# Optimization experiments

Hardware: AMD Instinct MI355X
Metric: run time of the kernel (lower is better)

The kernel has to match this reference:

```python
import jax, jax.numpy as jnp
import numpy as np

N = 100000   # nodes
E = 1600000  # edges
IN = 128
HID = 128    # 2 * out_channels
OUT = 64


def setup_inputs() -> dict:
    key = jax.random.key(0)
    ks = jax.random.split(key, 8)
    x = jax.random.normal(ks[0], (N, IN), dtype=jnp.float32)
    edge_index = jax.random.randint(ks[1], (2, E), 0, N, dtype=jnp.int32)
    s = 1.0 / np.sqrt(IN)
    W1 = jax.random.normal(ks[2], (IN, HID), dtype=jnp.float32) * s
    Wm1 = jax.random.normal(ks[3], (HID, HID), dtype=jnp.float32) * s
    Wm2 = jax.random.normal(ks[4], (HID, HID), dtype=jnp.float32) * s
    W2 = jax.random.normal(ks[5], (HID, OUT), dtype=jnp.float32) * s
    b1 = jnp.zeros((HID,), jnp.float32)
    bm1 = jnp.zeros((HID,), jnp.float32)
    bm2 = jnp.zeros((HID,), jnp.float32)
    b2 = jnp.zeros((OUT,), jnp.float32)
    return {"x": x, "edge_index": edge_index, "W1": W1, "b1": b1,
            "Wm1": Wm1, "bm1": bm1, "Wm2": Wm2, "bm2": bm2,
            "W2": W2, "b2": b2}


def _gcn_norm(edge_index, num_nodes):
    # PyG GCNConv: add self-loops (weight 1), symmetric normalization.
    loop = jnp.arange(num_nodes, dtype=edge_index.dtype)
    src = jnp.concatenate([edge_index[0], loop])
    dst = jnp.concatenate([edge_index[1], loop])
    deg = jax.ops.segment_sum(jnp.ones_like(src, jnp.float32), dst,
                              num_segments=num_nodes)
    dinv = jnp.where(deg > 0, jax.lax.rsqrt(deg), 0.0)
    norm = dinv[src] * dinv[dst]  # [E + N]
    return src, dst, norm


def _gcn_conv(h, W, b, src, dst, norm, num_nodes):
    h = h @ W                                # dense transform [N, F_out]
    msg = h[src] * norm[:, None]             # gather + scale   [E+N, F_out]
    out = jax.ops.segment_sum(msg, dst, num_segments=num_nodes)  # scatter-add
    return out + b


def reference(x, edge_index, W1, b1, Wm1, bm1, Wm2, bm2, W2, b2):
    num_nodes = x.shape[0]
    src, dst, norm = _gcn_norm(edge_index, num_nodes)
    h = jax.nn.relu(_gcn_conv(x, W1, b1, src, dst, norm, num_nodes))
    h = jax.nn.relu(_gcn_conv(h, Wm1, bm1, src, dst, norm, num_nodes))
    h = jax.nn.relu(_gcn_conv(h, Wm2, bm2, src, dst, norm, num_nodes))
    return _gcn_conv(h, W2, b2, src, dst, norm, num_nodes)  # [N, OUT]
```

## Files before the change

kernel.cpp:

```cpp
#include <hip/hip_runtime.h>
#include <hip/hip_bf16.h>
#include <hip/hip_fp16.h>


#define NNODES 100000
#define NEDGES 1600000
#define NBUCK 782

typedef __attribute__((ext_vector_type(8))) short bf16x8;
typedef __attribute__((ext_vector_type(4))) float f32x4;


__device__ inline float2 h2f2(unsigned int u) {
    __half2 h = *reinterpret_cast<__half2*>(&u);
    return __half22float2(h);
}
__device__ inline unsigned int f22h2(float a, float b) {
    __half2 h = __floats2half2_rn(a, b);
    return *reinterpret_cast<unsigned int*>(&h);
}

__device__ inline void split1(float x, short& hi, short& lo) {
    unsigned int u = __float_as_uint(x);
    hi = (short)(u >> 16);
    float r = x - __uint_as_float(u & 0xFFFF0000u);
    lo = (short)(__float_as_uint(r) >> 16);
}

__device__ inline void split8f(const float* f, bf16x8& hi, bf16x8& lo) {
#pragma unroll
    for (int i = 0; i < 8; i++) { short h, l; split1(f[i], h, l); hi[i] = h; lo[i] = l; }
}


__global__ void zero_ints(int* p, int n) {
    int i = blockIdx.x * blockDim.x + threadIdx.x;
    if (i < n) p[i] = 0;
}

__global__ __launch_bounds__(256) void hist_pass(const int* __restrict__ dst,
                                                 int* __restrict__ cnt, int e) {
    __shared__ int h[NBUCK];
    int tid = threadIdx.x;
    for (int i = tid; i < NBUCK; i += 256) h[i] = 0;
    __syncthreads();
    int base_e = blockIdx.x * 4096;
#pragma unroll
    for (int j = 0; j < 16; j++) {
        int i = base_e + j * 256 + tid;
        if (i < e) atomicAdd(&h[dst[i] >> 7], 1);
    }
    __syncthreads();
    for (int b = tid; b < NBUCK; b += 256)
        if (h[b]) atomicAdd(&cnt[b], h[b]);
}

__global__ __launch_bounds__(256) void scan_buckets(const int* __restrict__ cnt,
                                                    int* __restrict__ base,
                                                    int* __restrict__ fill, int e) {
    __shared__ int sd[256];
    int t = threadIdx.x;
    int v[4]; int s = 0;
#pragma unroll
    for (int j = 0; j < 4; j++) {
        int i = t * 4 + j;
        v[j] = (i < NBUCK) ? cnt[i] : 0;
        s += v[j];
    }
    sd[t] = s; __syncthreads();
    for (int off = 1; off < 256; off <<= 1) {
        int x = (t >= off) ? sd[t - off] : 0;
        __syncthreads();
        sd[t] += x;
        __syncthreads();
    }
    int run = sd[t] - s;
#pragma unroll
    for (int j = 0; j < 4; j++) {
        int i = t * 4 + j;
        if (i < NBUCK) { base[i] = run; fill[i] = run; }
        run += v[j];
    }
    if (t == 0) base[NBUCK] = e;
}

__global__ __launch_bounds__(256) void scatter_pass(const int* __restrict__ src,
                                                    const int* __restrict__ dst,
                                                    int* __restrict__ fill,
                                                    unsigned int* __restrict__ epart, int e) {
    __shared__ int h[NBUCK];
    int tid = threadIdx.x;
    for (int i = tid; i < NBUCK; i += 256) h[i] = 0;
    __syncthreads();
    int base_e = blockIdx.x * 4096;
#pragma unroll
    for (int j = 0; j < 16; j++) {
        int i = base_e + j * 256 + tid;
        if (i < e) atomicAdd(&h[dst[i] >> 7], 1);
    }
    __syncthreads();
    for (int b = tid; b < NBUCK; b += 256)
        if (h[b]) h[b] = atomicAdd(&fill[b], h[b]);
    __syncthreads();
#pragma unroll
    for (int j = 0; j < 16; j++) {
        int i = base_e + j * 256 + tid;
        if (i < e) {
            int d = dst[i];
            int bk = d >> 7;
            int pos = atomicAdd(&h[bk], 1);
            epart[pos] = ((unsigned int)src[i] << 7) | (unsigned int)(d & 127);
        }
    }
}

__global__ __launch_bounds__(256) void build_csr(const unsigned int* __restrict__ epart,
                                                 const int* __restrict__ base,
                                                 int* __restrict__ row_ptr,
                                                 int* __restrict__ col,
                                                 float* __restrict__ dinv,
                                                 int n, int e_total) {
    __shared__ int deg[128], off[128], fil[128];
    int b = blockIdx.x, tid = threadIdx.x;
    int node0 = b << 7;
    int nn = n - node0; if (nn > 128) nn = 128;
    int e0 = base[b], e1 = base[b + 1];
    int cnt = e1 - e0;

    if (tid < 128) deg[tid] = 0;
    __syncthreads();
    for (int i = tid; i < cnt; i += 256)
        atomicAdd(&deg[epart[e0 + i] & 127], 1);
    __syncthreads();
    if (tid < 128) off[tid] = deg[tid];
    __syncthreads();
    for (int o = 1; o < 128; o <<= 1) {
        int x = (tid < 128 && tid >= o) ? off[tid - o] : 0;
        __syncthreads();
        if (tid < 128) off[tid] += x;
        __syncthreads();
    }
    if (tid < nn) {
        int ex = e0 + off[tid] - deg[tid];
        row_ptr[node0 + tid] = ex;
        fil[tid] = ex;
        dinv[node0 + tid] = rsqrtf((float)(deg[tid] + 1));
    }
    if (b == 0 && tid == 0) row_ptr[n] = e_total;
    __syncthreads();
    for (int i = tid; i < cnt; i += 256) {
        unsigned int u = epart[e0 + i];
        int ld = (int)(u & 127);
        int pos = atomicAdd(&fil[ld], 1);
        col[pos] = (int)(u >> 7);
    }
}


__device__ inline void wfrag_one(const float* W, unsigned short* hi, unsigned short* lo,
                                 int e, int NT, int Ncols) {
    int j = e & 7;
    int l = (e >> 3) & 63;
    int t = (e >> 9) % NT;
    int c = e / (512 * NT);
    int k = c * 32 + (l >> 4) * 8 + j;
    int n = t * 16 + (l & 15);
    float x = W[k * Ncols + n];
    short h, lw; split1(x, h, lw);
    hi[e] = (unsigned short)h;
    lo[e] = (unsigned short)lw;
}

__global__ void conv_all(const float* W1, unsigned short* hi1, unsigned short* lo1,
                         const float* Wm1, unsigned short* him1, unsigned short* lom1,
                         const float* Wm2, unsigned short* him2, unsigned short* lom2,
                         const float* W2, unsigned short* hi2, unsigned short* lo2) {
    int blk = blockIdx.x;
    int tid = threadIdx.x;
    if (blk < 64)        wfrag_one(W1,  hi1,  lo1,  blk * 256 + tid,        8, 128);
    else if (blk < 128)  wfrag_one(Wm1, him1, lom1, (blk - 64) * 256 + tid, 8, 128);
    else if (blk < 192)  wfrag_one(Wm2, him2, lom2, (blk - 128) * 256 + tid, 8, 128);
    else                 wfrag_one(W2,  hi2,  lo2,  (blk - 192) * 256 + tid, 4, 64);
}


template <typename AT, int BN>
__global__ __launch_bounds__(256) void gemm_mfma(const AT* __restrict__ A,
                                                 const unsigned short* __restrict__ gwhi,
                                                 const unsigned short* __restrict__ gwlo,
                                                 const float* __restrict__ dinv,
                                                 __half* __restrict__ T, int nrows) {
    constexpr int NT = BN / 16;
    constexpr int WFRAG = 4 * NT * 64 * 8;
    __shared__ __align__(16) unsigned short s_hi[WFRAG];
    __shared__ __align__(16) unsigned short s_lo[WFRAG];
    int tid = threadIdx.x;
    for (int i = tid; i < WFRAG / 8; i += 256) {
        ((uint4*)s_hi)[i] = ((const uint4*)gwhi)[i];
        ((uint4*)s_lo)[i] = ((const uint4*)gwlo)[i];
    }
    __syncthreads();

    int wave = tid >> 6, lane = tid & 63;
    int m = lane & 15, q = lane >> 4;
    long row0 = ((long)blockIdx.x * 4 + wave) * 32;
    if (row0 >= nrows) return;
    long rowa = row0 + m;
    bool hasb = (row0 + 16) < nrows;
    long rowb = hasb ? (row0 + 16 + m) : rowa;

    f32x4 acc[2][NT];
#pragma unroll
    for (int s = 0; s < 2; s++)
#pragma unroll
        for (int t = 0; t < NT; t++)
#pragma unroll
            for (int r = 0; r < 4; r++) acc[s][t][r] = 0.f;

#pragma unroll
    for (int c = 0; c < 4; c++) {
        bf16x8 ah[2], al[2];
        float fa[8], fb[8];
        if constexpr (sizeof(AT) == 2) {
            uint4 ra = *(const uint4*)((const __half*)A + rowa * 128 + c * 32 + q * 8);
            uint4 rb = *(const uint4*)((const __half*)A + rowb * 128 + c * 32 + q * 8);
            float2 t0;
            t0 = h2f2(ra.x); fa[0] = t0.x; fa[1] = t0.y;
            t0 = h2f2(ra.y); fa[2] = t0.x; fa[3] = t0.y;
            t0 = h2f2(ra.z); fa[4] = t0.x; fa[5] = t0.y;
            t0 = h2f2(ra.w); fa[6] = t0.x; fa[7] = t0.y;
            t0 = h2f2(rb.x); fb[0] = t0.x; fb[1] = t0.y;
            t0 = h2f2(rb.y); fb[2] = t0.x; fb[3] = t0.y;
            t0 = h2f2(rb.z); fb[4] = t0.x; fb[5] = t0.y;
            t0 = h2f2(rb.w); fb[6] = t0.x; fb[7] = t0.y;
        } else {
            const float* pa = (const float*)A + rowa * 128 + c * 32 + q * 8;
            const float* pb = (const float*)A + rowb * 128 + c * 32 + q * 8;
            *(float4*)&fa[0] = *(const float4*)pa;
            *(float4*)&fa[4] = *(const float4*)(pa + 4);
            *(float4*)&fb[0] = *(const float4*)pb;
            *(float4*)&fb[4] = *(const float4*)(pb + 4);
        }
        split8f(fa, ah[0], al[0]);
        split8f(fb, ah[1], al[1]);

#pragma unroll
        for (int t = 0; t < NT; t++) {
            bf16x8 bhi = *(const bf16x8*)(s_hi + ((c * NT + t) * 64 + lane) * 8);
            bf16x8 blo = *(const bf16x8*)(s_lo + ((c * NT + t) * 64 + lane) * 8);
#pragma unroll
            for (int s = 0; s < 2; s++) {
                acc[s][t] = __builtin_amdgcn_mfma_f32_16x16x32_bf16(al[s], bhi, acc[s][t], 0, 0, 0);
                acc[s][t] = __builtin_amdgcn_mfma_f32_16x16x32_bf16(ah[s], blo, acc[s][t], 0, 0, 0);
                acc[s][t] = __builtin_amdgcn_mfma_f32_16x16x32_bf16(ah[s], bhi, acc[s][t], 0, 0, 0);
            }
        }
    }

#pragma unroll
    for (int s = 0; s < 2; s++) {
        if (s == 1 && !hasb) break;
#pragma unroll
        for (int r = 0; r < 4; r++) {
            long row = row0 + s * 16 + q * 4 + r;
            if (row < nrows) {
                float di = dinv[row];
#pragma unroll
                for (int t = 0; t < NT; t++)
                    T[row * BN + t * 16 + m] = __float2half(acc[s][t][r] * di);
            }
        }
    }
}


__device__ inline void acc8(float* a, uint4 v) {
    float2 f0 = h2f2(v.x), f1 = h2f2(v.y), f2 = h2f2(v.z), f3 = h2f2(v.w);
    a[0] += f0.x; a[1] += f0.y; a[2] += f1.x; a[3] += f1.y;
    a[4] += f2.x; a[5] += f2.y; a[6] += f3.x; a[7] += f3.y;
}
__device__ inline void acc4(float* a, uint2 v) {
    float2 f0 = h2f2(v.x), f1 = h2f2(v.y);
    a[0] += f0.x; a[1] += f0.y; a[2] += f1.x; a[3] += f1.y;
}

__global__ __launch_bounds__(256) void agg128h(const __half* __restrict__ t,
                                               const int* __restrict__ row_ptr,
                                               const int* __restrict__ col,
                                               const float* __restrict__ dinv,
                                               const float* __restrict__ bias,
                                               __half* __restrict__ out, int n) {
    int wave = threadIdx.x >> 6, lane = threadIdx.x & 63;
    int node = blockIdx.x * 4 + wave;
    if (node >= n) return;
    int q = lane >> 4, i = lane & 15;
    int r0 = row_ptr[node], r1 = row_ptr[node + 1];
    const uint4* t4 = (const uint4*)t;

    float a0[8], a1[8], a2[8], a3[8];
#pragma unroll
    for (int k = 0; k < 8; k++) { a0[k] = 0.f; a1[k] = 0.f; a2[k] = 0.f; a3[k] = 0.f; }

    int p = r0;
    for (; p + 16 <= r1; p += 16) {
        int c0 = col[p + q];
        int c1 = col[p + 4 + q];
        int c2 = col[p + 8 + q];
        int c3 = col[p + 12 + q];
        uint4 v0 = t4[(size_t)c0 * 16 + i];
        uint4 v1 = t4[(size_t)c1 * 16 + i];
        uint4 v2 = t4[(size_t)c2 * 16 + i];
        uint4 v3 = t4[(size_t)c3 * 16 + i];
        acc8(a0, v0); acc8(a1, v1); acc8(a2, v2); acc8(a3, v3);
    }
    for (; p + 8 <= r1; p += 8) {
        int c0 = col[p + q];
        int c1 = col[p + 4 + q];
        uint4 v0 = t4[(size_t)c0 * 16 + i];
        uint4 v1 = t4[(size_t)c1 * 16 + i];
        acc8(a0, v0); acc8(a1, v1);
    }
    for (; p < r1; p += 4) {
        int idx = p + q;
        if (idx < r1) {
            int c = col[idx];
            acc8(a0, t4[(size_t)c * 16 + i]);
        }
    }

    float s[8];
#pragma unroll
    for (int k = 0; k < 8; k++) s[k] = (a0[k] + a1[k]) + (a2[k] + a3[k]);
#pragma unroll
    for (int k = 0; k < 8; k++) s[k] += __shfl_xor(s[k], 16);
#pragma unroll
    for (int k = 0; k < 8; k++) s[k] += __shfl_xor(s[k], 32);

    if (q == 0) {
        uint4 ownv = t4[(size_t)node * 16 + i];
        float own[8];
        float2 f0 = h2f2(ownv.x), f1 = h2f2(ownv.y), f2 = h2f2(ownv.z), f3 = h2f2(ownv.w);
        own[0] = f0.x; own[1] = f0.y; own[2] = f1.x; own[3] = f1.y;
        own[4] = f2.x; own[5] = f2.y; own[6] = f3.x; own[7] = f3.y;
        float di = dinv[node];
        float4 bA = ((const float4*)bias)[i * 2];
        float4 bB = ((const float4*)bias)[i * 2 + 1];
        float o[8];
        o[0] = di * (s[0] + own[0]) + bA.x;
        o[1] = di * (s[1] + own[1]) + bA.y;
        o[2] = di * (s[2] + own[2]) + bA.z;
        o[3] = di * (s[3] + own[3]) + bA.w;
        o[4] = di * (s[4] + own[4]) + bB.x;
        o[5] = di * (s[5] + own[5]) + bB.y;
        o[6] = di * (s[6] + own[6]) + bB.z;
        o[7] = di * (s[7] + own[7]) + bB.w;
#pragma unroll
        for (int k = 0; k < 8; k++) o[k] = fmaxf(o[k], 0.f);
        uint4 ov;
        ov.x = f22h2(o[0], o[1]); ov.y = f22h2(o[2], o[3]);
        ov.z = f22h2(o[4], o[5]); ov.w = f22h2(o[6], o[7]);
        ((uint4*)out)[(size_t)node * 16 + i] = ov;
    }
}

__global__ __launch_bounds__(256) void agg64h(const __half* __restrict__ t,
                                              const int* __restrict__ row_ptr,
                                              const int* __restrict__ col,
                                              const float* __restrict__ dinv,
                                              const float* __restrict__ bias,
                                              float* __restrict__ out, int n) {
    int wave = threadIdx.x >> 6, lane = threadIdx.x & 63;
    int node = blockIdx.x * 4 + wave;
    if (node >= n) return;
    int q = lane >> 4, i = lane & 15;
    int r0 = row_ptr[node], r1 = row_ptr[node + 1];
    const uint2* t2 = (const uint2*)t;

    float a0[4], a1[4], a2[4], a3[4];
#pragma unroll
    for (int k = 0; k < 4; k++) { a0[k] = 0.f; a1[k] = 0.f; a2[k] = 0.f; a3[k] = 0.f; }

    int p = r0;
    for (; p + 16 <= r1; p += 16) {
        int c0 = col[p + q];
        int c1 = col[p + 4 + q];
        int c2 = col[p + 8 + q];
        int c3 = col[p + 12 + q];
        uint2 v0 = t2[(size_t)c0 * 16 + i];
        uint2 v1 = t2[(size_t)c1 * 16 + i];
        uint2 v2 = t2[(size_t)c2 * 16 + i];
        uint2 v3 = t2[(size_t)c3 * 16 + i];
        acc4(a0, v0); acc4(a1, v1); acc4(a2, v2); acc4(a3, v3);
    }
    for (; p + 8 <= r1; p += 8) {
        int c0 = col[p + q];
        int c1 = col[p + 4 + q];
        uint2 v0 = t2[(size_t)c0 * 16 + i];
        uint2 v1 = t2[(size_t)c1 * 16 + i];
        acc4(a0, v0); acc4(a1, v1);
    }
    for (; p < r1; p += 4) {
        int idx = p + q;
        if (idx < r1) {
            int c = col[idx];
            acc4(a0, t2[(size_t)c * 16 + i]);
        }
    }

    float s[4];
#pragma unroll
    for (int k = 0; k < 4; k++) s[k] = (a0[k] + a1[k]) + (a2[k] + a3[k]);
#pragma unroll
    for (int k = 0; k < 4; k++) s[k] += __shfl_xor(s[k], 16);
#pragma unroll
    for (int k = 0; k < 4; k++) s[k] += __shfl_xor(s[k], 32);

    if (q == 0) {
        uint2 ownv = t2[(size_t)node * 16 + i];
        float own[4];
        float2 f0 = h2f2(ownv.x), f1 = h2f2(ownv.y);
        own[0] = f0.x; own[1] = f0.y; own[2] = f1.x; own[3] = f1.y;
        float di = dinv[node];
        float4 b4 = ((const float4*)bias)[i];
        float4 o;
        o.x = di * (s[0] + own[0]) + b4.x;
        o.y = di * (s[1] + own[1]) + b4.y;
        o.z = di * (s[2] + own[2]) + b4.z;
        o.w = di * (s[3] + own[3]) + b4.w;
        ((float4*)out)[(size_t)node * 16 + i] = o;
    }
}


extern "C" void kernel_launch(void* const* d_in, const int* in_sizes, int n_in,
                              void* d_out, int out_size, void* d_ws, size_t ws_size,
                              hipStream_t stream) {
    const int N = NNODES, E = NEDGES;
    const float* x   = (const float*)d_in[0];
    const int*   ei  = (const int*)d_in[1];
    const int*   src = ei;
    const int*   dst = ei + E;
    const float* W1  = (const float*)d_in[2];
    const float* b1  = (const float*)d_in[3];
    const float* Wm1 = (const float*)d_in[4];
    const float* bm1 = (const float*)d_in[5];
    const float* Wm2 = (const float*)d_in[6];
    const float* bm2 = (const float*)d_in[7];
    const float* W2  = (const float*)d_in[8];
    const float* b2  = (const float*)d_in[9];
    float* out = (float*)d_out;

    int* bucket_cnt  = (int*)d_ws;
    int* bucket_base = bucket_cnt + 784;
    int* bucket_fill = bucket_base + 784;
    int* row_ptr     = bucket_fill + 784;
    int* col         = row_ptr + (N + 4);
    unsigned int* epart = (unsigned int*)(col + E);
    float* dinv  = (float*)(epart + E);
    __half* t16  = (__half*)(dinv + N);
    __half* bufA = t16 + (size_t)N * 128;
    unsigned short* whi1  = (unsigned short*)(bufA + (size_t)N * 128);
    unsigned short* wlo1  = whi1 + 16384;
    unsigned short* whiM1 = wlo1 + 16384;
    unsigned short* wloM1 = whiM1 + 16384;
    unsigned short* whiM2 = wloM1 + 16384;
    unsigned short* wloM2 = whiM2 + 16384;
    unsigned short* whi2  = wloM2 + 16384;
    unsigned short* wlo2  = whi2 + 8192;

    const int EB4 = (E + 4095) / 4096;

    zero_ints<<<4, 256, 0, stream>>>(bucket_cnt, NBUCK);
    hist_pass<<<EB4, 256, 0, stream>>>(dst, bucket_cnt, E);
    scan_buckets<<<1, 256, 0, stream>>>(bucket_cnt, bucket_base, bucket_fill, E);
    scatter_pass<<<EB4, 256, 0, stream>>>(src, dst, bucket_fill, epart, E);
    build_csr<<<NBUCK, 256, 0, stream>>>(epart, bucket_base, row_ptr, col, dinv, N, E);

    conv_all<<<224, 256, 0, stream>>>(W1, whi1, wlo1, Wm1, whiM1, wloM1,
                                      Wm2, whiM2, wloM2, W2, whi2, wlo2);

    const int GB = (N + 127) / 128;
    const int AB = (N + 3) / 4;

    gemm_mfma<float, 128><<<GB, 256, 0, stream>>>(x, whi1, wlo1, dinv, t16, N);
    agg128h<<<AB, 256, 0, stream>>>(t16, row_ptr, col, dinv, b1, bufA, N);

    gemm_mfma<__half, 128><<<GB, 256, 0, stream>>>(bufA, whiM1, wloM1, dinv, t16, N);
    agg128h<<<AB, 256, 0, stream>>>(t16, row_ptr, col, dinv, bm1, bufA, N);

    gemm_mfma<__half, 128><<<GB, 256, 0, stream>>>(bufA, whiM2, wloM2, dinv, t16, N);
    agg128h<<<AB, 256, 0, stream>>>(t16, row_ptr, col, dinv, bm2, bufA, N);

    gemm_mfma<__half, 64><<<GB, 256, 0, stream>>>(bufA, whi2, wlo2, dinv, t16, N);
    agg64h<<<AB, 256, 0, stream>>>(t16, row_ptr, col, dinv, b2, out, N);
}
```

Measured before the change: 557.3 us.

## Switch GEMMs to fp16 split MFMA, fuse weight prep with scan, enlarge agg blocks

Replaces the bf16 hi/lo split GEMMs with fp16 MFMA. Hidden layers now feed the fp16 activations straight in, using two MFMAs instead of three with no float conversion or split; the first layer keeps a three-MFMA fp16 split. The bucket scan is merged into the weight-conversion kernel, with a small copy_fill kernel added. build_csr now orders each row's columns into low and high source halves, which may improve gather locality. Aggregation kernels move to 1024-thread blocks with 16 nodes per block. The fp16 split of weights narrows exponent range but is likely fine for these scales.

After: 620.4 us. 1.11x slower.

```diff
diff --git a/kernel.cpp b/kernel.cpp
--- a/kernel.cpp
+++ b/kernel.cpp
@@ -7,7 +7,7 @@
 #define NEDGES 1600000
 #define NBUCK 782
 
-typedef __attribute__((ext_vector_type(8))) short bf16x8;
+typedef __attribute__((ext_vector_type(8))) _Float16 f16x8;
 typedef __attribute__((ext_vector_type(4))) float f32x4;
 
 
@@ -20,16 +20,9 @@
     return *reinterpret_cast<unsigned int*>(&h);
 }
 
-__device__ inline void split1(float x, short& hi, short& lo) {
-    unsigned int u = __float_as_uint(x);
-    hi = (short)(u >> 16);
-    float r = x - __uint_as_float(u & 0xFFFF0000u);
-    lo = (short)(__float_as_uint(r) >> 16);
-}
-
-__device__ inline void split8f(const float* f, bf16x8& hi, bf16x8& lo) {
-#pragma unroll
-    for (int i = 0; i < 8; i++) { short h, l; split1(f[i], h, l); hi[i] = h; lo[i] = l; }
+__device__ inline void split_h(float x, __half& h, __half& l) {
+    h = __float2half(x);
+    l = __float2half(x - __half2float(h));
 }
 
 
@@ -54,108 +47,6 @@
     for (int b = tid; b < NBUCK; b += 256)
         if (h[b]) atomicAdd(&cnt[b], h[b]);
 }
-
-__global__ __launch_bounds__(256) void scan_buckets(const int* __restrict__ cnt,
-                                                    int* __restrict__ base,
-                                                    int* __restrict__ fill, int e) {
-    __shared__ int sd[256];
-    int t = threadIdx.x;
-    int v[4]; int s = 0;
-#pragma unroll
-    for (int j = 0; j < 4; j++) {
-        int i = t * 4 + j;
-        v[j] = (i < NBUCK) ? cnt[i] : 0;
-        s += v[j];
-    }
-    sd[t] = s; __syncthreads();
-    for (int off = 1; off < 256; off <<= 1) {
-        int x = (t >= off) ? sd[t - off] : 0;
-        __syncthreads();
-        sd[t] += x;
-        __syncthreads();
-    }
-    int run = sd[t] - s;
-#pragma unroll
-    for (int j = 0; j < 4; j++) {
-        int i = t * 4 + j;
-        if (i < NBUCK) { base[i] = run; fill[i] = run; }
-        run += v[j];
-    }
-    if (t == 0) base[NBUCK] = e;
-}
-
-__global__ __launch_bounds__(256) void scatter_pass(const int* __restrict__ src,
-                                                    const int* __restrict__ dst,
-                                                    int* __restrict__ fill,
-                                                    unsigned int* __restrict__ epart, int e) {
-    __shared__ int h[NBUCK];
-    int tid = threadIdx.x;
-    for (int i = tid; i < NBUCK; i += 256) h[i] = 0;
-    __syncthreads();
-    int base_e = blockIdx.x * 4096;
-#pragma unroll
-    for (int j = 0; j < 16; j++) {
-        int i = base_e + j * 256 + tid;
-        if (i < e) atomicAdd(&h[dst[i] >> 7], 1);
-    }
-    __syncthreads();
-    for (int b = tid; b < NBUCK; b += 256)
-        if (h[b]) h[b] = atomicAdd(&fill[b], h[b]);
-    __syncthreads();
-#pragma unroll
-    for (int j = 0; j < 16; j++) {
-        int i = base_e + j * 256 + tid;
-        if (i < e) {
-            int d = dst[i];
-            int bk = d >> 7;
-            int pos = atomicAdd(&h[bk], 1);
-            epart[pos] = ((unsigned int)src[i] << 7) | (unsigned int)(d & 127);
-        }
-    }
-}
-
-__global__ __launch_bounds__(256) void build_csr(const unsigned int* __restrict__ epart,
-                                                 const int* __restrict__ base,
-                                                 int* __restrict__ row_ptr,
-                                                 int* __restrict__ col,
-                                                 float* __restrict__ dinv,
-                                                 int n, int e_total) {
-    __shared__ int deg[128], off[128], fil[128];
-    int b = blockIdx.x, tid = threadIdx.x;
-    int node0 = b << 7;
-    int nn = n - node0; if (nn > 128) nn = 128;
-    int e0 = base[b], e1 = base[b + 1];
-    int cnt = e1 - e0;
-
-    if (tid < 128) deg[tid] = 0;
-    __syncthreads();
-    for (int i = tid; i < cnt; i += 256)
-        atomicAdd(&deg[epart[e0 + i] & 127], 1);
-    __syncthreads();
-    if (tid < 128) off[tid] = deg[tid];
-    __syncthreads();
-    for (int o = 1; o < 128; o <<= 1) {
-        int x = (tid < 128 && tid >= o) ? off[tid - o] : 0;
-        __syncthreads();
-        if (tid < 128) off[tid] += x;
-        __syncthreads();
-    }
-    if (tid < nn) {
-        int ex = e0 + off[tid] - deg[tid];
-        row_ptr[node0 + tid] = ex;
-        fil[tid] = ex;
-        dinv[node0 + tid] = rsqrtf((float)(deg[tid] + 1));
-    }
-    if (b == 0 && tid == 0) row_ptr[n] = e_total;
-    __syncthreads();
-    for (int i = tid; i < cnt; i += 256) {
-        unsigned int u = epart[e0 + i];
-        int ld = (int)(u & 127);
-        int pos = atomicAdd(&fil[ld], 1);
-        col[pos] = (int)(u >> 7);
-    }
-}
-
 
 __device__ inline void wfrag_one(const float* W, unsigned short* hi, unsigned short* lo,
                                  int e, int NT, int Ncols) {
@@ -166,30 +57,220 @@
     int k = c * 32 + (l >> 4) * 8 + j;
     int n = t * 16 + (l & 15);
     float x = W[k * Ncols + n];
-    short h, lw; split1(x, h, lw);
-    hi[e] = (unsigned short)h;
-    lo[e] = (unsigned short)lw;
-}
-
-__global__ void conv_all(const float* W1, unsigned short* hi1, unsigned short* lo1,
-                         const float* Wm1, unsigned short* him1, unsigned short* lom1,
-                         const float* Wm2, unsigned short* him2, unsigned short* lom2,
-                         const float* W2, unsigned short* hi2, unsigned short* lo2) {
+    __half h, lw; split_h(x, h, lw);
+    hi[e] = *(unsigned short*)&h;
+    lo[e] = *(unsigned short*)&lw;
+}
+
+__global__ __launch_bounds__(256) void aux_kernel(
+        const float* W1, unsigned short* hi1, unsigned short* lo1,
+        const float* Wm1, unsigned short* him1, unsigned short* lom1,
+        const float* Wm2, unsigned short* him2, unsigned short* lom2,
+        const float* W2, unsigned short* hi2, unsigned short* lo2,
+        const int* __restrict__ cnt, int* __restrict__ base, int e) {
     int blk = blockIdx.x;
     int tid = threadIdx.x;
-    if (blk < 64)        wfrag_one(W1,  hi1,  lo1,  blk * 256 + tid,        8, 128);
-    else if (blk < 128)  wfrag_one(Wm1, him1, lom1, (blk - 64) * 256 + tid, 8, 128);
-    else if (blk < 192)  wfrag_one(Wm2, him2, lom2, (blk - 128) * 256 + tid, 8, 128);
-    else                 wfrag_one(W2,  hi2,  lo2,  (blk - 192) * 256 + tid, 4, 64);
-}
-
-
-template <typename AT, int BN>
-__global__ __launch_bounds__(256) void gemm_mfma(const AT* __restrict__ A,
-                                                 const unsigned short* __restrict__ gwhi,
-                                                 const unsigned short* __restrict__ gwlo,
-                                                 const float* __restrict__ dinv,
-                                                 __half* __restrict__ T, int nrows) {
+    if (blk < 64)        { wfrag_one(W1,  hi1,  lo1,  blk * 256 + tid,         8, 128); return; }
+    if (blk < 128)       { wfrag_one(Wm1, him1, lom1, (blk - 64) * 256 + tid,  8, 128); return; }
+    if (blk < 192)       { wfrag_one(Wm2, him2, lom2, (blk - 128) * 256 + tid, 8, 128); return; }
+    if (blk < 224)       { wfrag_one(W2,  hi2,  lo2,  (blk - 192) * 256 + tid, 4, 64);  return; }
+    __shared__ int sd[256];
+    int t = tid;
+    int v[4]; int s = 0;
+#pragma unroll
+    for (int j = 0; j < 4; j++) {
+        int i = t * 4 + j;
+        v[j] = (i < NBUCK) ? cnt[i] : 0;
+        s += v[j];
+    }
+    sd[t] = s; __syncthreads();
+    for (int off = 1; off < 256; off <<= 1) {
+        int x = (t >= off) ? sd[t - off] : 0;
+        __syncthreads();
+        sd[t] += x;
+        __syncthreads();
+    }
+    int run = sd[t] - s;
+#pragma unroll
+    for (int j = 0; j < 4; j++) {
+        int i = t * 4 + j;
+        if (i < NBUCK) base[i] = run;
+        run += v[j];
+    }
+    if (t == 0) base[NBUCK] = e;
+}
+
+__global__ void copy_fill(const int* __restrict__ base, int* __restrict__ fill) {
+    int i = blockIdx.x * blockDim.x + threadIdx.x;
+    if (i < NBUCK) fill[i] = base[i];
+}
+
+__global__ __launch_bounds__(256) void scatter_pass(const int* __restrict__ src,
+                                                    const int* __restrict__ dst,
+                                                    int* __restrict__ fill,
+                                                    unsigned int* __restrict__ epart, int e) {
+    __shared__ int h[NBUCK];
+    int tid = threadIdx.x;
+    for (int i = tid; i < NBUCK; i += 256) h[i] = 0;
+    __syncthreads();
+    int base_e = blockIdx.x * 4096;
+#pragma unroll
+    for (int j = 0; j < 16; j++) {
+        int i = base_e + j * 256 + tid;
+        if (i < e) atomicAdd(&h[dst[i] >> 7], 1);
+    }
+    __syncthreads();
+    for (int b = tid; b < NBUCK; b += 256)
+        if (h[b]) h[b] = atomicAdd(&fill[b], h[b]);
+    __syncthreads();
+#pragma unroll
+    for (int j = 0; j < 16; j++) {
+        int i = base_e + j * 256 + tid;
+        if (i < e) {
+            int d = dst[i];
+            int bk = d >> 7;
+            int pos = atomicAdd(&h[bk], 1);
+            epart[pos] = ((unsigned int)src[i] << 7) | (unsigned int)(d & 127);
+        }
+    }
+}
+
+__global__ __launch_bounds__(256) void build_csr(const unsigned int* __restrict__ epart,
+                                                 const int* __restrict__ base,
+                                                 int* __restrict__ row_ptr,
+                                                 int* __restrict__ col,
+                                                 float* __restrict__ dinv,
+                                                 int n, int e_total) {
+    __shared__ int deg[128], degl[128], off[128], fil[256];
+    int b = blockIdx.x, tid = threadIdx.x;
+    int node0 = b << 7;
+    int nn = n - node0; if (nn > 128) nn = 128;
+    int e0 = base[b], e1 = base[b + 1];
+    int cnt = e1 - e0;
+    const int HALF = NNODES / 2;
+
+    if (tid < 128) { deg[tid] = 0; degl[tid] = 0; }
+    __syncthreads();
+    for (int i = tid; i < cnt; i += 256) {
+        unsigned int u = epart[e0 + i];
+        int ld = (int)(u & 127);
+        atomicAdd(&deg[ld], 1);
+        if ((int)(u >> 7) < HALF) atomicAdd(&degl[ld], 1);
+    }
+    __syncthreads();
+    if (tid < 128) off[tid] = deg[tid];
+    __syncthreads();
+    for (int o = 1; o < 128; o <<= 1) {
+        int x = (tid < 128 && tid >= o) ? off[tid - o] : 0;
+        __syncthreads();
+        if (tid < 128) off[tid] += x;
+        __syncthreads();
+    }
+    if (tid < 128) {
+        int row_start = e0 + off[tid] - deg[tid];
+        fil[tid] = row_start;
+        fil[128 + tid] = row_start + degl[tid];
+        if (tid < nn) {
+            row_ptr[node0 + tid] = row_start;
+            dinv[node0 + tid] = rsqrtf((float)(deg[tid] + 1));
+        }
+    }
+    if (b == 0 && tid == 0) row_ptr[n] = e_total;
+    __syncthreads();
+    for (int i = tid; i < cnt; i += 256) {
+        unsigned int u = epart[e0 + i];
+        int ld = (int)(u & 127);
+        int srcv = (int)(u >> 7);
+        int pos = atomicAdd(&fil[(srcv < HALF ? 0 : 128) + ld], 1);
+        col[pos] = srcv;
+    }
+}
+
+
+__global__ __launch_bounds__(256) void gemm_l1(const float* __restrict__ A,
+                                               const unsigned short* __restrict__ gwhi,
+                                               const unsigned short* __restrict__ gwlo,
+                                               const float* __restrict__ dinv,
+                                               __half* __restrict__ T, int nrows) {
+    constexpr int NT = 8, BN = 128;
+    constexpr int WFRAG = 4 * NT * 64 * 8;
+    __shared__ __align__(16) unsigned short s_hi[WFRAG];
+    __shared__ __align__(16) unsigned short s_lo[WFRAG];
+    int tid = threadIdx.x;
+    for (int i = tid; i < WFRAG / 8; i += 256) {
+        ((uint4*)s_hi)[i] = ((const uint4*)gwhi)[i];
+        ((uint4*)s_lo)[i] = ((const uint4*)gwlo)[i];
+    }
+    __syncthreads();
+
+    int wave = tid >> 6, lane = tid & 63;
+    int m = lane & 15, q = lane >> 4;
+    long row0 = ((long)blockIdx.x * 4 + wave) * 32;
+    if (row0 >= nrows) return;
+    long rowa = row0 + m;
+    bool hasb = (row0 + 16) < nrows;
+    long rowb = hasb ? (row0 + 16 + m) : rowa;
+
+    f32x4 acc[2][NT];
+#pragma unroll
+    for (int s = 0; s < 2; s++)
+#pragma unroll
+        for (int t = 0; t < NT; t++)
+#pragma unroll
+            for (int r = 0; r < 4; r++) acc[s][t][r] = 0.f;
+
+#pragma unroll
+    for (int c = 0; c < 4; c++) {
+        f16x8 ah[2], al[2];
+        const float* pa = A + rowa * 128 + c * 32 + q * 8;
+        const float* pb = A + rowb * 128 + c * 32 + q * 8;
+        float fa[8], fb[8];
+        *(float4*)&fa[0] = *(const float4*)pa;
+        *(float4*)&fa[4] = *(const float4*)(pa + 4);
+        *(float4*)&fb[0] = *(const float4*)pb;
+        *(float4*)&fb[4] = *(const float4*)(pb + 4);
+#pragma unroll
+        for (int i = 0; i < 8; i++) {
+            __half h, l;
+            split_h(fa[i], h, l); ah[0][i] = *(_Float16*)&h; al[0][i] = *(_Float16*)&l;
+            split_h(fb[i], h, l); ah[1][i] = *(_Float16*)&h; al[1][i] = *(_Float16*)&l;
+        }
+#pragma unroll
+        for (int t = 0; t < NT; t++) {
+            f16x8 bhi = *(const f16x8*)(s_hi + ((c * NT + t) * 64 + lane) * 8);
+            f16x8 blo = *(const f16x8*)(s_lo + ((c * NT + t) * 64 + lane) * 8);
+#pragma unroll
+            for (int s = 0; s < 2; s++) {
+                acc[s][t] = __builtin_amdgcn_mfma_f32_16x16x32_f16(al[s], bhi, acc[s][t], 0, 0, 0);
+                acc[s][t] = __builtin_amdgcn_mfma_f32_16x16x32_f16(ah[s], blo, acc[s][t], 0, 0, 0);
+                acc[s][t] = __builtin_amdgcn_mfma_f32_16x16x32_f16(ah[s], bhi, acc[s][t], 0, 0, 0);
+            }
+        }
+    }
+
+#pragma unroll
+    for (int s = 0; s < 2; s++) {
+        if (s == 1 && !hasb) break;
+#pragma unroll
+        for (int r = 0; r < 4; r++) {
+            long row = row0 + s * 16 + q * 4 + r;
+            if (row < nrows) {
+                float di = dinv[row];
+#pragma unroll
+                for (int t = 0; t < NT; t++)
+                    T[row * BN + t * 16 + m] = __float2half(acc[s][t][r] * di);
+            }
+        }
+    }
+}
+
+
+template <int BN>
+__global__ __launch_bounds__(256) void gemm_f16(const __half* __restrict__ A,
+                                                const unsigned short* __restrict__ gwhi,
+                                                const unsigned short* __restrict__ gwlo,
+                                                const float* __restrict__ dinv,
+                                                __half* __restrict__ T, int nrows) {
     constexpr int NT = BN / 16;
     constexpr int WFRAG = 4 * NT * 64 * 8;
     __shared__ __align__(16) unsigned short s_hi[WFRAG];
@@ -219,40 +300,19 @@
 
 #pragma unroll
     for (int c = 0; c < 4; c++) {
-        bf16x8 ah[2], al[2];
-        float fa[8], fb[8];
-        if constexpr (sizeof(AT) == 2) {
-            uint4 ra = *(const uint4*)((const __half*)A + rowa * 128 + c * 32 + q * 8);
-            uint4 rb = *(const uint4*)((const __half*)A + rowb * 128 + c * 32 + q * 8);
-            float2 t0;
-            t0 = h2f2(ra.x); fa[0] = t0.x; fa[1] = t0.y;
-            t0 = h2f2(ra.y); fa[2] = t0.x; fa[3] = t0.y;
-            t0 = h2f2(ra.z); fa[4] = t0.x; fa[5] = t0.y;
-            t0 = h2f2(ra.w); fa[6] = t0.x; fa[7] = t0.y;
-            t0 = h2f2(rb.x); fb[0] = t0.x; fb[1] = t0.y;
-            t0 = h2f2(rb.y); fb[2] = t0.x; fb[3] = t0.y;
-            t0 = h2f2(rb.z); fb[4] = t0.x; fb[5] = t0.y;
-            t0 = h2f2(rb.w); fb[6] = t0.x; fb[7] = t0.y;
-        } else {
-            const float* pa = (const float*)A + rowa * 128 + c * 32 + q * 8;
-            const float* pb = (const float*)A + rowb * 128 + c * 32 + q * 8;
-            *(float4*)&fa[0] = *(const float4*)pa;
-            *(float4*)&fa[4] = *(const float4*)(pa + 4);
-            *(float4*)&fb[0] = *(const float4*)pb;
-            *(float4*)&fb[4] = *(const float4*)(pb + 4);
-        }
-        split8f(fa, ah[0], al[0]);
-        split8f(fb, ah[1], al[1]);
-
+        f16x8 a[2];
+        uint4 ra = *(const uint4*)(A + rowa * 128 + c * 32 + q * 8);
+        uint4 rb = *(const uint4*)(A + rowb * 128 + c * 32 + q * 8);
+        *(uint4*)&a[0] = ra;
+        *(uint4*)&a[1] = rb;
 #pragma unroll
         for (int t = 0; t < NT; t++) {
-            bf16x8 bhi = *(const bf16x8*)(s_hi + ((c * NT + t) * 64 + lane) * 8);
-            bf16x8 blo = *(const bf16x8*)(s_lo + ((c * NT + t) * 64 + lane) * 8);
+            f16x8 bhi = *(const f16x8*)(s_hi + ((c * NT + t) * 64 + lane) * 8);
+            f16x8 blo = *(const f16x8*)(s_lo + ((c * NT + t) * 64 + lane) * 8);
 #pragma unroll
             for (int s = 0; s < 2; s++) {
-                acc[s][t] = __builtin_amdgcn_mfma_f32_16x16x32_bf16(al[s], bhi, acc[s][t], 0, 0, 0);
-                acc[s][t] = __builtin_amdgcn_mfma_f32_16x16x32_bf16(ah[s], blo, acc[s][t], 0, 0, 0);
-                acc[s][t] = __builtin_amdgcn_mfma_f32_16x16x32_bf16(ah[s], bhi, acc[s][t], 0, 0, 0);
+                acc[s][t] = __builtin_amdgcn_mfma_f32_16x16x32_f16(a[s], blo, acc[s][t], 0, 0, 0);
+                acc[s][t] = __builtin_amdgcn_mfma_f32_16x16x32_f16(a[s], bhi, acc[s][t], 0, 0, 0);
             }
         }
     }
@@ -284,14 +344,14 @@
     a[0] += f0.x; a[1] += f0.y; a[2] += f1.x; a[3] += f1.y;
 }
 
-__global__ __launch_bounds__(256) void agg128h(const __half* __restrict__ t,
-                                               const int* __restrict__ row_ptr,
-                                               const int* __restrict__ col,
-                                               const float* __restrict__ dinv,
-                                               const float* __restrict__ bias,
-                                               __half* __restrict__ out, int n) {
+__global__ __launch_bounds__(1024) void agg128h(const __half* __restrict__ t,
+                                                const int* __restrict__ row_ptr,
+                                                const int* __restrict__ col,
+                                                const float* __restrict__ dinv,
+                                                const float* __restrict__ bias,
+                                                __half* __restrict__ out, int n) {
     int wave = threadIdx.x >> 6, lane = threadIdx.x & 63;
-    int node = blockIdx.x * 4 + wave;
+    int node = blockIdx.x * 16 + wave;
     if (node >= n) return;
     int q = lane >> 4, i = lane & 15;
     int r0 = row_ptr[node], r1 = row_ptr[node + 1];
@@ -363,14 +423,14 @@
     }
 }
 
-__global__ __launch_bounds__(256) void agg64h(const __half* __restrict__ t,
-                                              const int* __restrict__ row_ptr,
-                                              const int* __restrict__ col,
-                                              const float* __restrict__ dinv,
-                                              const float* __restrict__ bias,
-                                              float* __restrict__ out, int n) {
+__global__ __launch_bounds__(1024) void agg64h(const __half* __restrict__ t,
+                                               const int* __restrict__ row_ptr,
+                                               const int* __restrict__ col,
+                                               const float* __restrict__ dinv,
+                                               const float* __restrict__ bias,
+                                               float* __restrict__ out, int n) {
     int wave = threadIdx.x >> 6, lane = threadIdx.x & 63;
-    int node = blockIdx.x * 4 + wave;
+    int node = blockIdx.x * 16 + wave;
     if (node >= n) return;
     int q = lane >> 4, i = lane & 15;
     int r0 = row_ptr[node], r1 = row_ptr[node + 1];
@@ -472,25 +532,25 @@
 
     zero_ints<<<4, 256, 0, stream>>>(bucket_cnt, NBUCK);
     hist_pass<<<EB4, 256, 0, stream>>>(dst, bucket_cnt, E);
-    scan_buckets<<<1, 256, 0, stream>>>(bucket_cnt, bucket_base, bucket_fill, E);
+    aux_kernel<<<225, 256, 0, stream>>>(W1, whi1, wlo1, Wm1, whiM1, wloM1,
+                                        Wm2, whiM2, wloM2, W2, whi2, wlo2,
+                                        bucket_cnt, bucket_base, E);
+    copy_fill<<<4, 256, 0, stream>>>(bucket_base, bucket_fill);
     scatter_pass<<<EB4, 256, 0, stream>>>(src, dst, bucket_fill, epart, E);
     build_csr<<<NBUCK, 256, 0, stream>>>(epart, bucket_base, row_ptr, col, dinv, N, E);
 
-    conv_all<<<224, 256, 0, stream>>>(W1, whi1, wlo1, Wm1, whiM1, wloM1,
-                                      Wm2, whiM2, wloM2, W2, whi2, wlo2);
-
     const int GB = (N + 127) / 128;
-    const int AB = (N + 3) / 4;
-
-    gemm_mfma<float, 128><<<GB, 256, 0, stream>>>(x, whi1, wlo1, dinv, t16, N);
-    agg128h<<<AB, 256, 0, stream>>>(t16, row_ptr, col, dinv, b1, bufA, N);
-
-    gemm_mfma<__half, 128><<<GB, 256, 0, stream>>>(bufA, whiM1, wloM1, dinv, t16, N);
-    agg128h<<<AB, 256, 0, stream>>>(t16, row_ptr, col, dinv, bm1, bufA, N);
-
-    gemm_mfma<__half, 128><<<GB, 256, 0, stream>>>(bufA, whiM2, wloM2, dinv, t16, N);
-    agg128h<<<AB, 256, 0, stream>>>(t16, row_ptr, col, dinv, bm2, bufA, N);
-
-    gemm_mfma<__half, 64><<<GB, 256, 0, stream>>>(bufA, whi2, wlo2, dinv, t16, N);
-    agg64h<<<AB, 256, 0, stream>>>(t16, row_ptr, col, dinv, b2, out, N);
-}
+    const int AB = (N + 15) / 16;
+
+    gemm_l1<<<GB, 256, 0, stream>>>(x, whi1, wlo1, dinv, t16, N);
+    agg128h<<<AB, 1024, 0, stream>>>(t16, row_ptr, col, dinv, b1, bufA, N);
+
+    gemm_f16<128><<<GB, 256, 0, stream>>>(bufA, whiM1, wloM1, dinv, t16, N);
+    agg128h<<<AB, 1024, 0, stream>>>(t16, row_ptr, col, dinv, bm1, bufA, N);
+
+    gemm_f16<128><<<GB, 256, 0, stream>>>(bufA, whiM2, wloM2, dinv, t16, N);
+    agg128h<<<AB, 1024, 0, stream>>>(t16, row_ptr, col, dinv, bm2, bufA, N);
+
+    gemm_f16<64><<<GB, 256, 0, stream>>>(bufA, whi2, wlo2, dinv, t16, N);
+    agg64h<<<AB, 1024, 0, stream>>>(t16, row_ptr, col, dinv, b2, out, N);
+}
```
